# Kernel tuning notes

Hardware: AMD Instinct MI355X
Metric: run time of the kernel (lower is better)

Reference implementation:

```python
import jax, jax.numpy as jnp
import numpy as np


def conv1d(x, w, b, pad):
    # x: (B, Cin, T), w: (Cout, Cin, K), b: (Cout,)
    y = jax.lax.conv_general_dilated(x, w, window_strides=(1,), padding=[(pad, pad)],
                                     dimension_numbers=('NCH', 'OIH', 'NCH'))
    return y + b[None, :, None]


def setup_inputs() -> dict:
    key = jax.random.key(0)
    ks = jax.random.split(key, 12)
    B, Cm, T1, Ct, T2, Ca = 8, 80, 800, 512, 200, 80
    queries = jax.random.normal(ks[0], (B, Cm, T1), dtype=jnp.float32)
    keys = jax.random.normal(ks[1], (B, Ct, T2), dtype=jnp.float32)
    query_lens = jnp.full((B,), T1, dtype=jnp.int32)
    key_lens = jax.random.randint(ks[2], (B,), T2 // 2, T2 + 1)
    # mask True where key position is padding (>= key_len): (B, T2, 1)
    mask = (jnp.arange(T2)[None, :] >= key_lens[:, None])[:, :, None]
    attn_prior = jax.random.uniform(ks[3], (B, T1, T2), dtype=jnp.float32) + 0.1
    # key_proj: Conv1d(512->1024, k=3, pad=1) + ReLU + Conv1d(1024->80, k=1)
    kp_w1 = jax.random.normal(ks[4], (2 * Ct, Ct, 3), jnp.float32) * 0.02
    kp_b1 = jnp.zeros((2 * Ct,), jnp.float32)
    kp_w2 = jax.random.normal(ks[5], (Ca, 2 * Ct, 1), jnp.float32) * 0.02
    kp_b2 = jnp.zeros((Ca,), jnp.float32)
    # query_proj (3xconv): Conv1d(80->160,k3)+ReLU+Conv1d(160->80,k1)+ReLU+Conv1d(80->80,k1)
    qp_w1 = jax.random.normal(ks[6], (2 * Cm, Cm, 3), jnp.float32) * 0.05
    qp_b1 = jnp.zeros((2 * Cm,), jnp.float32)
    qp_w2 = jax.random.normal(ks[7], (Cm, 2 * Cm, 1), jnp.float32) * 0.05
    qp_b2 = jnp.zeros((Cm,), jnp.float32)
    qp_w3 = jax.random.normal(ks[8], (Ca, Cm, 1), jnp.float32) * 0.05
    qp_b3 = jnp.zeros((Ca,), jnp.float32)
    return {"queries": queries, "keys": keys, "query_lens": query_lens, "mask": mask,
            "attn_prior": attn_prior, "kp_w1": kp_w1, "kp_b1": kp_b1, "kp_w2": kp_w2,
            "kp_b2": kp_b2, "qp_w1": qp_w1, "qp_b1": qp_b1, "qp_w2": qp_w2,
            "qp_b2": qp_b2, "qp_w3": qp_w3, "qp_b3": qp_b3}


def reference(queries, keys, query_lens, mask, attn_prior,
              kp_w1, kp_b1, kp_w2, kp_b2,
              qp_w1, qp_b1, qp_w2, qp_b2, qp_w3, qp_b3):
    # key projection: (B, Ct, T2) -> (B, Ca, T2)
    ke = conv1d(keys, kp_w1, kp_b1, pad=1)
    ke = jax.nn.relu(ke)
    ke = conv1d(ke, kp_w2, kp_b2, pad=0)
    # query projection ('3xconv'): (B, Cm, T1) -> (B, Ca, T1)
    qe = conv1d(queries, qp_w1, qp_b1, pad=1)
    qe = jax.nn.relu(qe)
    qe = conv1d(qe, qp_w2, qp_b2, pad=0)
    qe = jax.nn.relu(qe)
    qe = conv1d(qe, qp_w3, qp_b3, pad=0)
    # broadcasted squared L2 distance: (B, Ca, T1, T2) -> reduce C -> (B, 1, T1, T2)
    diff2 = (qe[:, :, :, None] - ke[:, :, None, :]) ** 2
    attn = -0.0005 * jnp.sum(diff2, axis=1, keepdims=True)
    # prior in log domain
    attn = jax.nn.log_softmax(attn, axis=3) + jnp.log(attn_prior[:, None] + 1e-8)
    attn_logprob = attn
    # mask (B, T2, 1) -> (B, 1, 1, T2)
    m = jnp.transpose(mask, (0, 2, 1))[:, :, None, :]
    attn = jnp.where(m, -jnp.inf, attn)
    attn = jax.nn.softmax(attn, axis=3)
    return (attn, attn_logprob)
```

## Files before the change

### kernel.cpp

```cpp
#include <hip/hip_runtime.h>
#include <hip/hip_bf16.h>
#include <math.h>

#define B_  8
#define CM  80
#define T1_ 800
#define CT  512
#define T2_ 200
#define CA  80

using bf16 = __hip_bfloat16;
typedef __attribute__((ext_vector_type(8))) short bf16x8;
typedef __attribute__((ext_vector_type(4))) float f32x4;

#define LDSW 56
#define LDSW2 72
#define LDSW3 168
#define LDSW4 104

__device__ __forceinline__ float load_sel(const void* p, long idx, int isf32) {
  if (isf32) return ((const float*)p)[idx];
  return __bfloat162float(((const bf16*)p)[idx]);
}

__device__ __forceinline__ unsigned short f2bf(float x) {
  bf16 h = __float2bfloat16(x);
  return *reinterpret_cast<unsigned short*>(&h);
}

__device__ __forceinline__ int detect_f32(const unsigned short* q) {
  __shared__ int s_f;
  const int tid = threadIdx.x;
  if (tid < 64) {
    unsigned short u = q[2 * tid];
    int e = (u >> 7) & 0xFF;
    unsigned long long bal = __ballot(e < 100 || e > 154);
    if (tid == 0) s_f = (__popcll(bal) >= 16) ? 1 : 0;
  }
  __syncthreads();
  return s_f;
}

__device__ void task_cvt_t(const void* X, bf16* XT, int f, int C, int T,
                           int id2, int tilesT, float* smem, int tid) {
  const int per_b = tilesT * ((C + 31) >> 5);
  const int b = id2 / per_b;
  const int r = id2 - b * per_b;
  const int ct = r / tilesT, tt = r - ct * tilesT;
  const int c0 = ct * 32, t0 = tt * 32;
  const int tx = tid & 31, trow = tid >> 5;
#pragma unroll
  for (int p = 0; p < 4; ++p) {
    const int cr = trow + 8 * p;
    if (c0 + cr < C && t0 + tx < T)
      smem[cr * 33 + tx] = load_sel(X, ((long)b * C + c0 + cr) * T + t0 + tx, f);
  }
  __syncthreads();
#pragma unroll
  for (int p = 0; p < 4; ++p) {
    const int tr = trow + 8 * p;
    if (t0 + tr < T && c0 + tx < C)
      XT[((long)b * T + t0 + tr) * C + c0 + tx] =
          __float2bfloat16(smem[tx * 33 + tr]);
  }
}

__device__ void task_wfrag(const void* W, bf16* WF, int f, int id2, int tid) {
  const int id = id2 * 256 + tid;
  const int l  = id & 63;
  int rest = id >> 6;
  const int h  = rest & 1; rest >>= 1;
  const int mi = rest & 3; rest >>= 2;
  const int w2 = rest & 1; rest >>= 1;
  const int ks = rest % 24;
  const int p  = rest / 24;
  const int co = p * 128 + w2 * 64 + mi * 16 + (l & 15);
  const int k0 = ks * 64 + h * 32 + (l >> 4) * 8;
  const int dk = k0 >> 9;
  const int ci = k0 & 511;
  const long sbase = ((long)co * 512 + ci) * 3 + dk;
  ushort4 u0, u1;
  u0.x = f2bf(load_sel(W, sbase + 0 * 3, f));
  u0.y = f2bf(load_sel(W, sbase + 1 * 3, f));
  u0.z = f2bf(load_sel(W, sbase + 2 * 3, f));
  u0.w = f2bf(load_sel(W, sbase + 3 * 3, f));
  u1.x = f2bf(load_sel(W, sbase + 4 * 3, f));
  u1.y = f2bf(load_sel(W, sbase + 5 * 3, f));
  u1.z = f2bf(load_sel(W, sbase + 6 * 3, f));
  u1.w = f2bf(load_sel(W, sbase + 7 * 3, f));
  *(ushort4*)(WF + (long)id * 8) = u0;
  *(ushort4*)(WF + (long)id * 8 + 4) = u1;
}

__device__ void task_wt3v(const void* W, bf16* WT, int f, int Co, int Ci,
                          int id2, int tid) {
  const int i = id2 * 256 + tid;
  const int g4 = Ci >> 2;
  if (i >= Co * g4) return;
  const int co = i / g4, ci = (i - co * g4) * 4;
  const long sbase = ((long)co * Ci + ci) * 3;
  float w[12];
  if (f) {
    const float4* s = (const float4*)((const float*)W + sbase);
    float4 f0 = s[0], f1 = s[1], f2 = s[2];
    w[0]=f0.x; w[1]=f0.y; w[2]=f0.z; w[3]=f0.w; w[4]=f1.x; w[5]=f1.y;
    w[6]=f1.z; w[7]=f1.w; w[8]=f2.x; w[9]=f2.y; w[10]=f2.z; w[11]=f2.w;
  } else {
#pragma unroll
    for (int j = 0; j < 12; ++j) w[j] = load_sel(W, sbase + j, 0);
  }
#pragma unroll
  for (int dk = 0; dk < 3; ++dk) {
    ushort4 u;
    u.x = f2bf(w[0 * 3 + dk]); u.y = f2bf(w[1 * 3 + dk]);
    u.z = f2bf(w[2 * 3 + dk]); u.w = f2bf(w[3 * 3 + dk]);
    *(ushort4*)(WT + ((long)dk * Co + co) * Ci + ci) = u;
  }
}

__device__ void task_cvtv(const void* W, bf16* O, int f, int n, int id2, int tid) {
  const int i = (id2 * 256 + tid) * 4;
  if (i >= n) return;
  ushort4 u;
  if (f) {
    float4 v = *(const float4*)((const float*)W + i);
    u.x = f2bf(v.x); u.y = f2bf(v.y); u.z = f2bf(v.z); u.w = f2bf(v.w);
  } else {
    u.x = f2bf(load_sel(W, i, 0));     u.y = f2bf(load_sel(W, i + 1, 0));
    u.z = f2bf(load_sel(W, i + 2, 0)); u.w = f2bf(load_sel(W, i + 3, 0));
  }
  *(ushort4*)(O + i) = u;
}

__global__ __launch_bounds__(256) void k_prep(
    const void* __restrict__ queries, const void* __restrict__ keys,
    const void* __restrict__ mask,
    const void* __restrict__ kp_w1, const void* __restrict__ kp_b1,
    const void* __restrict__ kp_w2, const void* __restrict__ kp_b2,
    const void* __restrict__ qp_w1, const void* __restrict__ qp_b1,
    const void* __restrict__ qp_w2, const void* __restrict__ qp_b2,
    const void* __restrict__ qp_w3, const void* __restrict__ qp_b3,
    bf16* __restrict__ keysT, bf16* __restrict__ queriesT,
    bf16* __restrict__ w1F, bf16* __restrict__ qw1T,
    bf16* __restrict__ kw2c, bf16* __restrict__ qw2c, bf16* __restrict__ qw3c,
    float* __restrict__ biasf, float* __restrict__ mf, float* __restrict__ kn) {
  __shared__ float smem[32 * 33];
  const int tid = threadIdx.x;
  const int f = detect_f32((const unsigned short*)queries);
  int id = blockIdx.x;

  if (id < 896) { task_cvt_t(keys, keysT, f, CT, T2_, id, 7, smem, tid); return; }
  id -= 896;
  if (id < 600) { task_cvt_t(queries, queriesT, f, CM, T1_, id, 25, smem, tid); return; }
  id -= 600;
  if (id < 768) { task_wfrag(kp_w1, w1F, f, id, tid); return; }
  id -= 768;
  if (id < 13) { task_wt3v(qp_w1, qw1T, f, 160, CM, id, tid); return; }
  id -= 13;
  if (id < 80) { task_cvtv(kp_w2, kw2c, f, 80 * 1024, id, tid); return; }
  id -= 80;
  if (id < 13) { task_cvtv(qp_w2, qw2c, f, 80 * 160, id, tid); return; }
  id -= 13;
  if (id < 7) { task_cvtv(qp_w3, qw3c, f, 80 * 80, id, tid); return; }
  id -= 7;

  if (id == 0) {
    for (int i = tid; i < 1424; i += 256) {
      float v;
      if (i < 1024)      v = load_sel(kp_b1, i, f);
      else if (i < 1104) v = load_sel(kp_b2, i - 1024, f);
      else if (i < 1264) v = load_sel(qp_b1, i - 1104, f);
      else if (i < 1344) v = load_sel(qp_b2, i - 1264, f);
      else               v = load_sel(qp_b3, i - 1344, f);
      biasf[i] = v;
    }
    for (int i = tid; i < B_ * T2_; i += 256) kn[i] = 0.f;
    return;
  }

  {
    int* s_fmt = (int*)smem;
    const int nmask = B_ * T2_;
    if (tid == 0) s_fmt[0] = 1;
    __syncthreads();
    const unsigned int* wi = (const unsigned int*)mask;
    const int nw = nmask / 4;
    int pri = 0;
    for (int i = tid; i < nw; i += 256) {
      unsigned int w = wi[i];
      if (w == 0u || w == 1u) continue;
      if (w == 0x3F803F80u || w == 0x00003F80u) { pri = max(pri, 2); continue; }
      if (w == 0x3F800000u) continue;
      unsigned int b0 = w & 0xFFu, b1 = (w >> 8) & 0xFFu,
                   b2 = (w >> 16) & 0xFFu, b3 = (w >> 24) & 0xFFu;
      if (b0 <= 1u && b1 <= 1u && b2 <= 1u && b3 <= 1u) pri = max(pri, 3);
      else pri = max(pri, 2);
    }
    if (pri) atomicMax(&s_fmt[0], pri);
    __syncthreads();
    const int fmt = s_fmt[0];
    for (int i = tid; i < nmask; i += 256) {
      int m;
      if (fmt == 3)      m = ((const unsigned char*)mask)[i] != 0;
      else if (fmt == 2) m = ((const unsigned short*)mask)[i] != 0;
      else               m = (wi[i] != 0u);
      mf[i] = (float)m;
    }
  }
}

__device__ void conv_tile(
    const bf16* __restrict__ XT, const bf16* __restrict__ WT,
    const float* __restrict__ bias, void* __restrict__ Y,
    int Cin, int Cout, int T, int KW, int pad, int relu, int outmode,
    int m0, int n0, short* As, short* Bs, float* Y2 = nullptr) {
  const int K = Cin * KW;
  const int tid = threadIdx.x;
  const int wave = tid >> 6;
  const int lane = tid & 63;

  const int row = tid >> 2;
  const int koff = (tid & 3) * 8;
  const int n = n0 + row;
  const int bb = n / T;
  const int t = n - bb * T;

  const int wm = (wave >> 1) * 32;
  const int wn = (wave & 1) * 32;
  const int fm = lane & 15;
  const int quad = lane >> 4;

  f32x4 acc[2][2] = {};

  const short* ap0 = As + (wm + fm) * LDSW + quad * 8;
  const short* bp0 = Bs + (wn + fm) * LDSW + quad * 8;

  auto loadA = [&](int k0) -> uint4 {
    const int k = k0 + koff;
    const int m = m0 + row;
    uint4 v = {0u, 0u, 0u, 0u};
    if (m < Cout && k < K) {
      const int dk = k / Cin;
      const int ci = k - dk * Cin;
      v = *(const uint4*)(WT + ((long)dk * Cout + m) * Cin + ci);
    }
    return v;
  };
  auto loadB = [&](int k0) -> uint4 {
    const int k = k0 + koff;
    uint4 v = {0u, 0u, 0u, 0u};
    if (k < K) {
      const int dk = k / Cin;
      const int ci = k - dk * Cin;
      const int tt = t + dk - pad;
      if (tt >= 0 && tt < T)
        v = *(const uint4*)(XT + ((long)bb * T + tt) * Cin + ci);
    }
    return v;
  };

  uint4 va = loadA(0);
  uint4 vb = loadB(0);

  for (int k0 = 0; k0 < K; k0 += 32) {
    *(uint4*)(As + row * LDSW + koff) = va;
    *(uint4*)(Bs + row * LDSW + koff) = vb;
    if (k0 + 32 < K) {
      va = loadA(k0 + 32);
      vb = loadB(k0 + 32);
    }
    __syncthreads();
    {
      bf16x8 a0 = *(const bf16x8*)(ap0);
      bf16x8 a1 = *(const bf16x8*)(ap0 + 16 * LDSW);
      bf16x8 b0 = *(const bf16x8*)(bp0);
      bf16x8 b1 = *(const bf16x8*)(bp0 + 16 * LDSW);
      acc[0][0] = __builtin_amdgcn_mfma_f32_16x16x32_bf16(a0, b0, acc[0][0], 0, 0, 0);
      acc[0][1] = __builtin_amdgcn_mfma_f32_16x16x32_bf16(a0, b1, acc[0][1], 0, 0, 0);
      acc[1][0] = __builtin_amdgcn_mfma_f32_16x16x32_bf16(a1, b0, acc[1][0], 0, 0, 0);
      acc[1][1] = __builtin_amdgcn_mfma_f32_16x16x32_bf16(a1, b1, acc[1][1], 0, 0, 0);
    }
    __syncthreads();
  }

#pragma unroll
  for (int mi = 0; mi < 2; ++mi) {
    const int mrow = m0 + wm + mi * 16 + quad * 4;
    if (mrow >= Cout) continue;
    float bi[4];
#pragma unroll
    for (int r = 0; r < 4; ++r) bi[r] = bias[mrow + r];
#pragma unroll
    for (int ni = 0; ni < 2; ++ni) {
      const int ncol = n0 + wn + ni * 16 + fm;
      float o[4];
#pragma unroll
      for (int r = 0; r < 4; ++r) {
        float v = acc[mi][ni][r] + bi[r];
        if (relu) v = fmaxf(v, 0.f);
        o[r] = v;
      }
      if (outmode == 0) {
        ushort4 u;
        u.x = f2bf(o[0]); u.y = f2bf(o[1]); u.z = f2bf(o[2]); u.w = f2bf(o[3]);
        *(ushort4*)((bf16*)Y + (long)ncol * Cout + mrow) = u;
      } else if (outmode == 1) {
        *(float4*)((float*)Y + (long)ncol * Cout + mrow) =
            make_float4(o[0], o[1], o[2], o[3]);
      } else {
        const int bb2 = ncol / T;
        const int tloc = ncol - bb2 * T;
        float s4 = 0.f;
#pragma unroll
        for (int r = 0; r < 4; ++r) {
          ((float*)Y)[((long)bb2 * Cout + mrow + r) * T + tloc] = -2.f * o[r];
          s4 = fmaf(o[r], o[r], s4);
        }
        atomicAdd(&Y2[ncol], s4);
      }
    }
  }
}

__device__ void conv_key128(
    const bf16* __restrict__ XT, const bf16* __restrict__ WF,
    const float* __restrict__ bias, bf16* __restrict__ Y,
    int panel, int n0, short* Bs) {
  const int Cin = CT, Cout = 1024, T = T2_;
  const int tid = threadIdx.x;
  const int wave = tid >> 6;
  const int lane = tid & 63;
  const int m0 = panel * 128;

  const int rowb = tid >> 2;
  const int nb = n0 + rowb;
  const int bbb = nb / T;
  const int tb = nb - bbb * T;
  const int kcb = (tid & 3) * 16;

  const int w2 = wave >> 1;
  const int wm = w2 * 64;
  const int wn = (wave & 1) * 32;
  const int fm = lane & 15;
  const int quad = lane >> 4;

  f32x4 acc[4][2] = {};
  const short* bp0 = Bs + (wn + fm) * LDSW2 + quad * 8;

  uint4 vb0, vb1;
  auto loadB = [&](int k0) {
    const int dk = k0 >> 9;
    const int ci0 = k0 & 511;
    const int tt = tb + dk - 1;
    if (tt >= 0 && tt < T) {
      const bf16* src = XT + ((long)bbb * T + tt) * Cin + ci0 + kcb;
      vb0 = *(const uint4*)(src);
      vb1 = *(const uint4*)(src + 8);
    } else {
      uint4 z = {0u, 0u, 0u, 0u};
      vb0 = z; vb1 = z;
    }
  };

  loadB(0);

  for (int k0 = 0; k0 < 1536; k0 += 64) {
    const int ks = k0 >> 6;
    {
      short* dstb = Bs + rowb * LDSW2 + kcb;
      *(uint4*)(dstb) = vb0;
      *(uint4*)(dstb + 8) = vb1;
    }
    if (k0 + 64 < 1536) loadB(k0 + 64);

    const long abase = ((((long)panel * 24 + ks) * 2 + w2) * 4096) + lane * 8;
    bf16x8 a[4][2];
#pragma unroll
    for (int mi = 0; mi < 4; ++mi)
#pragma unroll
      for (int h = 0; h < 2; ++h)
        a[mi][h] = *(const bf16x8*)(WF + abase + (mi * 2 + h) * 512);

    __syncthreads();
#pragma unroll
    for (int h = 0; h < 2; ++h) {
      bf16x8 b0 = *(const bf16x8*)(bp0 + h * 32);
      bf16x8 b1 = *(const bf16x8*)(bp0 + 16 * LDSW2 + h * 32);
#pragma unroll
      for (int mi = 0; mi < 4; ++mi) {
        acc[mi][0] = __builtin_amdgcn_mfma_f32_16x16x32_bf16(a[mi][h], b0, acc[mi][0], 0, 0, 0);
        acc[mi][1] = __builtin_amdgcn_mfma_f32_16x16x32_bf16(a[mi][h], b1, acc[mi][1], 0, 0, 0);
      }
    }
    __syncthreads();
  }

#pragma unroll
  for (int mi = 0; mi < 4; ++mi) {
    const int mrow = m0 + wm + mi * 16 + quad * 4;
    float bi[4];
#pragma unroll
    for (int r = 0; r < 4; ++r) bi[r] = bias[mrow + r];
#pragma unroll
    for (int ni = 0; ni < 2; ++ni) {
      const int ncol = n0 + wn + ni * 16 + fm;
      const long base = (long)ncol * Cout + mrow;
      ushort4 u;
      u.x = f2bf(fmaxf(acc[mi][ni][0] + bi[0], 0.f));
      u.y = f2bf(fmaxf(acc[mi][ni][1] + bi[1], 0.f));
      u.z = f2bf(fmaxf(acc[mi][ni][2] + bi[2], 0.f));
      u.w = f2bf(fmaxf(acc[mi][ni][3] + bi[3], 0.f));
      *(ushort4*)(Y + base) = u;
    }
  }
}

__global__ __launch_bounds__(256) void k_conv1(
    const bf16* __restrict__ keysT, const bf16* __restrict__ w1F,
    const float* __restrict__ b_k1, bf16* __restrict__ ke1T,
    const bf16* __restrict__ queriesT, const bf16* __restrict__ qw1T,
    const float* __restrict__ b_q1, bf16* __restrict__ qe1T) {
  __shared__ __align__(16) short smem[2 * 64 * LDSW];
  int j = blockIdx.x;
  if (j < 200) {
    conv_key128(keysT, w1F, b_k1, ke1T, j & 7, (j >> 3) * 64, smem);
  } else {
    j -= 200;
    conv_tile(queriesT, qw1T, b_q1, qe1T, CM, 160, T1_, 3, 1, 1, 0,
              (j / 100) * 64, (j % 100) * 64, smem, smem + 64 * LDSW);
  }
}

__device__ void conv23_tile(
    const bf16* __restrict__ qe1T, const bf16* __restrict__ qw2c,
    const float* __restrict__ b_q2, const bf16* __restrict__ qw3c,
    const float* __restrict__ b_q3, float* __restrict__ qeT,
    float* __restrict__ qn, int n0, short* smem) {
  short* sIn = smem;
  short* sW2 = smem + 64 * LDSW3;
  short* sC  = smem;
  short* sW3 = smem + 64 * LDSW3;
  const int tid = threadIdx.x;
  const int wave = tid >> 6;
  const int lane = tid & 63;
  const int fm = lane & 15;
  const int quad = lane >> 4;

#pragma unroll
  for (int c = tid; c < 1280; c += 256) {
    const int row = c / 20, kc = (c - row * 20) * 8;
    uint4 v = *(const uint4*)(qe1T + (long)(n0 + row) * 160 + kc);
    *(uint4*)(sIn + row * LDSW3 + kc) = v;
  }
  for (int c = tid; c < 1600; c += 256) {
    const int row = c / 20, kc = (c - row * 20) * 8;
    uint4 v = *(const uint4*)(qw2c + (long)row * 160 + kc);
    *(uint4*)(sW2 + row * LDSW3 + kc) = v;
  }
  __syncthreads();

  f32x4 acc1[5] = {};
#pragma unroll
  for (int ks = 0; ks < 5; ++ks) {
    bf16x8 b = *(const bf16x8*)(sIn + (16 * wave + fm) * LDSW3 + ks * 32 + quad * 8);
#pragma unroll
    for (int mt = 0; mt < 5; ++mt) {
      bf16x8 a = *(const bf16x8*)(sW2 + (16 * mt + fm) * LDSW3 + ks * 32 + quad * 8);
      acc1[mt] = __builtin_amdgcn_mfma_f32_16x16x32_bf16(a, b, acc1[mt], 0, 0, 0);
    }
  }
  __syncthreads();

#pragma unroll
  for (int mt = 0; mt < 5; ++mt) {
    const int ch = 16 * mt + quad * 4;
    const float4 b2 = *(const float4*)(b_q2 + ch);
    ushort4 u;
    u.x = f2bf(fmaxf(acc1[mt][0] + b2.x, 0.f));
    u.y = f2bf(fmaxf(acc1[mt][1] + b2.y, 0.f));
    u.z = f2bf(fmaxf(acc1[mt][2] + b2.z, 0.f));
    u.w = f2bf(fmaxf(acc1[mt][3] + b2.w, 0.f));
    *(ushort4*)(sC + (16 * wave + fm) * LDSW4 + ch) = u;
  }
  if (tid < 128) {
    const int row = tid >> 1, off = 80 + (tid & 1) * 8;
    uint4 z = {0u, 0u, 0u, 0u};
    *(uint4*)(sC + row * LDSW4 + off) = z;
  }
  for (int c = tid; c < 800; c += 256) {
    const int row = c / 10, kc = (c - row * 10) * 8;
    uint4 v = *(const uint4*)(qw3c + (long)row * 80 + kc);
    *(uint4*)(sW3 + row * LDSW4 + kc) = v;
  }
  if (tid < 160) {
    const int row = tid >> 1, off = 80 + (tid & 1) * 8;
    uint4 z = {0u, 0u, 0u, 0u};
    *(uint4*)(sW3 + row * LDSW4 + off) = z;
  }
  __syncthreads();

  f32x4 acc2[5] = {};
#pragma unroll
  for (int ks = 0; ks < 3; ++ks) {
    bf16x8 b = *(const bf16x8*)(sC + (16 * wave + fm) * LDSW4 + ks * 32 + quad * 8);
#pragma unroll
    for (int mt = 0; mt < 5; ++mt) {
      bf16x8 a = *(const bf16x8*)(sW3 + (16 * mt + fm) * LDSW4 + ks * 32 + quad * 8);
      acc2[mt] = __builtin_amdgcn_mfma_f32_16x16x32_bf16(a, b, acc2[mt], 0, 0, 0);
    }
  }

  const int pos = n0 + 16 * wave + fm;
  float p = 0.f;
#pragma unroll
  for (int mt = 0; mt < 5; ++mt) {
    const int ch = 16 * mt + quad * 4;
    const float4 b3 = *(const float4*)(b_q3 + ch);
    float4 o = make_float4(acc2[mt][0] + b3.x, acc2[mt][1] + b3.y,
                           acc2[mt][2] + b3.z, acc2[mt][3] + b3.w);
    p = fmaf(o.x, o.x, p); p = fmaf(o.y, o.y, p);
    p = fmaf(o.z, o.z, p); p = fmaf(o.w, o.w, p);
    *(float4*)(qeT + (long)pos * CA + ch) = o;
  }
  p += __shfl_xor(p, 16, 64);
  p += __shfl_xor(p, 32, 64);
  if (quad == 0) qn[pos] = p;
}

__global__ __launch_bounds__(256) void k_conv2f(
    const bf16* __restrict__ ke1T, const bf16* __restrict__ kw2c,
    const float* __restrict__ b_k2, float* __restrict__ keT,
    float* __restrict__ kn,
    const bf16* __restrict__ qe1T, const bf16* __restrict__ qw2c,
    const float* __restrict__ b_q2, const bf16* __restrict__ qw3c,
    const float* __restrict__ b_q3, float* __restrict__ qeT,
    float* __restrict__ qn) {
  __shared__ __align__(16) short smem[64 * LDSW3 + 80 * LDSW3];
  int j = blockIdx.x;
  if (j < 50) {
    conv_tile(ke1T, kw2c, b_k2, keT, 1024, CA, T2_, 1, 0, 0, 2,
              (j / 25) * 64, (j % 25) * 64, smem, smem + 64 * LDSW, kn);
  } else {
    conv23_tile(qe1T, qw2c, b_q2, qw3c, b_q3, qeT, qn, (j - 50) * 64, smem);
  }
}

__global__ __launch_bounds__(256) void k_dist(
    const float* __restrict__ qeT, const float* __restrict__ keT2,
    const float* __restrict__ kn, const float* __restrict__ qn,
    const void* __restrict__ prior, const float* __restrict__ mf,
    void* __restrict__ out, const unsigned short* __restrict__ qprobe) {
  __shared__ float sq[4 * CA];
  __shared__ float sqn[4];
  __shared__ float redA[16], redB[16], redC[16], redD[16];
  const int f = detect_f32(qprobe);
  const int b = blockIdx.y;
  const int t1base = blockIdx.x * 4;
  const int tid = threadIdx.x;
  const int wid = tid >> 6;

  for (int i = tid; i < 4 * CA; i += 256) {
    int u = i / CA, c = i - u * CA;
    sq[i] = qeT[((long)b * T1_ + t1base + u) * CA + c];
  }
  if (tid < 4) sqn[tid] = qn[b * T1_ + t1base + tid];
  __syncthreads();

  const int t2 = tid;
  const bool valid = (t2 < T2_);
  float x[4] = {-INFINITY, -INFINITY, -INFINITY, -INFINITY};
  if (valid) {
    const float* kp = keT2 + (long)b * CA * T2_ + t2;
    const float knv = kn[b * T2_ + t2];
    float a0 = 0.f, a1 = 0.f, a2 = 0.f, a3 = 0.f;
#pragma unroll 2
    for (int j = 0; j < CA; j += 4) {
      const float4 q0 = *(const float4*)(sq + 0 * CA + j);
      const float4 q1 = *(const float4*)(sq + 1 * CA + j);
      const float4 q2 = *(const float4*)(sq + 2 * CA + j);
      const float4 q3 = *(const float4*)(sq + 3 * CA + j);
      const float k0v = kp[(j + 0) * T2_];
      const float k1v = kp[(j + 1) * T2_];
      const float k2v = kp[(j + 2) * T2_];
      const float k3v = kp[(j + 3) * T2_];
      a0 = fmaf(k0v, q0.x, a0); a0 = fmaf(k1v, q0.y, a0);
      a0 = fmaf(k2v, q0.z, a0); a0 = fmaf(k3v, q0.w, a0);
      a1 = fmaf(k0v, q1.x, a1); a1 = fmaf(k1v, q1.y, a1);
      a1 = fmaf(k2v, q1.z, a1); a1 = fmaf(k3v, q1.w, a1);
      a2 = fmaf(k0v, q2.x, a2); a2 = fmaf(k1v, q2.y, a2);
      a2 = fmaf(k2v, q2.z, a2); a2 = fmaf(k3v, q2.w, a2);
      a3 = fmaf(k0v, q3.x, a3); a3 = fmaf(k1v, q3.y, a3);
      a3 = fmaf(k2v, q3.z, a3); a3 = fmaf(k3v, q3.w, a3);
    }
    x[0] = -0.0005f * (a0 + sqn[0] + knv);
    x[1] = -0.0005f * (a1 + sqn[1] + knv);
    x[2] = -0.0005f * (a2 + sqn[2] + knv);
    x[3] = -0.0005f * (a3 + sqn[3] + knv);
  }

  const float mval = valid ? mf[b * T2_ + t2] : 0.f;
  const long N = (long)B_ * T1_ * T2_;

  float m[4] = {x[0], x[1], x[2], x[3]};
#pragma unroll
  for (int o = 32; o > 0; o >>= 1)
#pragma unroll
    for (int u = 0; u < 4; ++u) m[u] = fmaxf(m[u], __shfl_down(m[u], o, 64));
  if ((tid & 63) == 0)
#pragma unroll
    for (int u = 0; u < 4; ++u) redA[wid * 4 + u] = m[u];
  __syncthreads();
  float M1[4];
#pragma unroll
  for (int u = 0; u < 4; ++u)
    M1[u] = fmaxf(fmaxf(redA[u], redA[4 + u]), fmaxf(redA[8 + u], redA[12 + u]));

  float e[4], s1[4];
#pragma unroll
  for (int u = 0; u < 4; ++u) {
    e[u] = (x[u] == -INFINITY) ? 0.f : __expf(x[u] - M1[u]);
    s1[u] = e[u];
  }
#pragma unroll
  for (int o = 32; o > 0; o >>= 1)
#pragma unroll
    for (int u = 0; u < 4; ++u) s1[u] += __shfl_down(s1[u], o, 64);
  if ((tid & 63) == 0)
#pragma unroll
    for (int u = 0; u < 4; ++u) redB[wid * 4 + u] = s1[u];
  __syncthreads();
  float lp[4];
#pragma unroll
  for (int u = 0; u < 4; ++u) {
    const float S1 = redB[u] + redB[4 + u] + redB[8 + u] + redB[12 + u];
    const float logZ = __logf(S1);
    lp[u] = -INFINITY;
    if (valid) {
      const long oidx = ((long)b * T1_ + t1base + u) * T2_ + t2;
      float pr = load_sel(prior, oidx, f);
      lp[u] = (x[u] - M1[u] - logZ) + __logf(fmaxf(pr, 0.f) + 1e-8f);
      if (f) ((float*)out)[N + oidx] = lp[u];
      else   ((bf16*)out)[N + oidx] = __float2bfloat16(lp[u]);
    }
  }

  float xm[4], m2[4];
#pragma unroll
  for (int u = 0; u < 4; ++u) {
    xm[u] = (valid && mval != 0.f) ? -INFINITY : lp[u];
    m2[u] = xm[u];
  }
#pragma unroll
  for (int o = 32; o > 0; o >>= 1)
#pragma unroll
    for (int u = 0; u < 4; ++u) m2[u] = fmaxf(m2[u], __shfl_down(m2[u], o, 64));
  if ((tid & 63) == 0)
#pragma unroll
    for (int u = 0; u < 4; ++u) redC[wid * 4 + u] = m2[u];
  __syncthreads();
  float M2[4];
#pragma unroll
  for (int u = 0; u < 4; ++u)
    M2[u] = fmaxf(fmaxf(redC[u], redC[4 + u]), fmaxf(redC[8 + u], redC[12 + u]));

  float e2[4], s2[4];
#pragma unroll
  for (int u = 0; u < 4; ++u) {
    e2[u] = (xm[u] == -INFINITY) ? 0.f : __expf(xm[u] - M2[u]);
    s2[u] = e2[u];
  }
#pragma unroll
  for (int o = 32; o > 0; o >>= 1)
#pragma unroll
    for (int u = 0; u < 4; ++u) s2[u] += __shfl_down(s2[u], o, 64);
  if ((tid & 63) == 0)
#pragma unroll
    for (int u = 0; u < 4; ++u) redD[wid * 4 + u] = s2[u];
  __syncthreads();
#pragma unroll
  for (int u = 0; u < 4; ++u) {
    const float S2 = redD[u] + redD[4 + u] + redD[8 + u] + redD[12 + u];
    if (valid) {
      float a = (S2 > 0.f) ? (e2[u] / S2) : 0.f;
      const long oidx = ((long)b * T1_ + t1base + u) * T2_ + t2;
      if (f) ((float*)out)[oidx] = a;
      else   ((bf16*)out)[oidx] = __float2bfloat16(a);
    }
  }
}

extern "C" void kernel_launch(void* const* d_in, const int* in_sizes, int n_in,
                              void* d_out, int out_size, void* d_ws, size_t ws_size,
                              hipStream_t stream) {
  const void* queries = d_in[0];
  const void* keys    = d_in[1];
  const void* mask    = d_in[3];
  const void* prior   = d_in[4];
  const void* kp_w1 = d_in[5];
  const void* kp_b1 = d_in[6];
  const void* kp_w2 = d_in[7];
  const void* kp_b2 = d_in[8];
  const void* qp_w1 = d_in[9];
  const void* qp_b1 = d_in[10];
  const void* qp_w2 = d_in[11];
  const void* qp_b2 = d_in[12];
  const void* qp_w3 = d_in[13];
  const void* qp_b3 = d_in[14];

  float* keT   = (float*)d_ws;
  float* qeT   = keT + 128000;
  float* mf    = qeT + 512000;
  float* biasf = mf + 1600;
  float* kn    = biasf + 1440;
  float* qn    = kn + 1600;
  bf16* keysT    = (bf16*)(qn + 6400);
  bf16* queriesT = keysT + 819200;
  bf16* w1F      = queriesT + 512000;
  bf16* qw1T     = w1F + 1572864;
  bf16* kw2c     = qw1T + 38400;
  bf16* qw2c     = kw2c + 81920;
  bf16* qw3c     = qw2c + 12800;
  bf16* ke1T     = qw3c + 6400;
  bf16* qe1T     = ke1T + 1638400;

  float* b_k1 = biasf;
  float* b_k2 = biasf + 1024;
  float* b_q1 = biasf + 1104;
  float* b_q2 = biasf + 1264;
  float* b_q3 = biasf + 1344;

  k_prep<<<2379, 256, 0, stream>>>(
      queries, keys, mask,
      kp_w1, kp_b1, kp_w2, kp_b2,
      qp_w1, qp_b1, qp_w2, qp_b2, qp_w3, qp_b3,
      keysT, queriesT, w1F, qw1T, kw2c, qw2c, qw3c, biasf, mf, kn);

  k_conv1<<<500, 256, 0, stream>>>(keysT, w1F, b_k1, ke1T,
                                   queriesT, qw1T, b_q1, qe1T);

  k_conv2f<<<150, 256, 0, stream>>>(ke1T, kw2c, b_k2, keT, kn,
                                    qe1T, qw2c, b_q2, qw3c, b_q3, qeT, qn);

  k_dist<<<dim3(200, B_), 256, 0, stream>>>(
      qeT, keT, kn, qn, prior, mf, d_out, (const unsigned short*)queries);
}
```

Baseline: 150.8 us.

## Prefetch weight fragments across K-steps and merge softmax reductions in dist kernel

In the key conv GEMM, the A (weight) fragments for the next K-step are now loaded into a second register set while the current step's MFMAs run, overlapping global loads with compute at the cost of extra VGPRs. In the distance kernel, the prior and mask loads move to the start of the kernel. The second softmax is rewritten algebraically: its logsumexp shift cancels, so it runs on x plus log-prior directly. This lets the two max reductions and the two sum reductions each run together, cutting the block barriers from four to two. The change risks register pressure in the conv kernel and slight numerical differences in the softmax.

```diff
diff --git a/kernel.cpp b/kernel.cpp
--- a/kernel.cpp
+++ b/kernel.cpp
@@ -339,7 +339,6 @@
   const int kcb = (tid & 3) * 16;
 
   const int w2 = wave >> 1;
-  const int wm = w2 * 64;
   const int wn = (wave & 1) * 32;
   const int fm = lane & 15;
   const int quad = lane >> 4;
@@ -362,42 +361,57 @@
     }
   };
 
+  bf16x8 a0c[4], a1c[4], a0n[4], a1n[4];
+  auto loadA = [&](int ks, bf16x8 d0[4], bf16x8 d1[4]) {
+    const long abase = ((((long)panel * 24 + ks) * 2 + w2) * 4096) + lane * 8;
+#pragma unroll
+    for (int mi = 0; mi < 4; ++mi) {
+      d0[mi] = *(const bf16x8*)(WF + abase + (mi * 2 + 0) * 512);
+      d1[mi] = *(const bf16x8*)(WF + abase + (mi * 2 + 1) * 512);
+    }
+  };
+
   loadB(0);
+  loadA(0, a0c, a1c);
 
   for (int k0 = 0; k0 < 1536; k0 += 64) {
-    const int ks = k0 >> 6;
     {
       short* dstb = Bs + rowb * LDSW2 + kcb;
       *(uint4*)(dstb) = vb0;
       *(uint4*)(dstb + 8) = vb1;
     }
-    if (k0 + 64 < 1536) loadB(k0 + 64);
-
-    const long abase = ((((long)panel * 24 + ks) * 2 + w2) * 4096) + lane * 8;
-    bf16x8 a[4][2];
-#pragma unroll
-    for (int mi = 0; mi < 4; ++mi)
-#pragma unroll
-      for (int h = 0; h < 2; ++h)
-        a[mi][h] = *(const bf16x8*)(WF + abase + (mi * 2 + h) * 512);
-
+    const bool more = (k0 + 64 < 1536);
+    if (more) {
+      loadB(k0 + 64);
+      loadA((k0 >> 6) + 1, a0n, a1n);
+    }
     __syncthreads();
-#pragma unroll
-    for (int h = 0; h < 2; ++h) {
-      bf16x8 b0 = *(const bf16x8*)(bp0 + h * 32);
-      bf16x8 b1 = *(const bf16x8*)(bp0 + 16 * LDSW2 + h * 32);
+    {
+      bf16x8 b00 = *(const bf16x8*)(bp0);
+      bf16x8 b01 = *(const bf16x8*)(bp0 + 16 * LDSW2);
 #pragma unroll
       for (int mi = 0; mi < 4; ++mi) {
-        acc[mi][0] = __builtin_amdgcn_mfma_f32_16x16x32_bf16(a[mi][h], b0, acc[mi][0], 0, 0, 0);
-        acc[mi][1] = __builtin_amdgcn_mfma_f32_16x16x32_bf16(a[mi][h], b1, acc[mi][1], 0, 0, 0);
+        acc[mi][0] = __builtin_amdgcn_mfma_f32_16x16x32_bf16(a0c[mi], b00, acc[mi][0], 0, 0, 0);
+        acc[mi][1] = __builtin_amdgcn_mfma_f32_16x16x32_bf16(a0c[mi], b01, acc[mi][1], 0, 0, 0);
       }
+      bf16x8 b10 = *(const bf16x8*)(bp0 + 32);
+      bf16x8 b11 = *(const bf16x8*)(bp0 + 16 * LDSW2 + 32);
+#pragma unroll
+      for (int mi = 0; mi < 4; ++mi) {
+        acc[mi][0] = __builtin_amdgcn_mfma_f32_16x16x32_bf16(a1c[mi], b10, acc[mi][0], 0, 0, 0);
+        acc[mi][1] = __builtin_amdgcn_mfma_f32_16x16x32_bf16(a1c[mi], b11, acc[mi][1], 0, 0, 0);
+      }
     }
     __syncthreads();
+    if (more) {
+#pragma unroll
+      for (int mi = 0; mi < 4; ++mi) { a0c[mi] = a0n[mi]; a1c[mi] = a1n[mi]; }
+    }
   }
 
 #pragma unroll
   for (int mi = 0; mi < 4; ++mi) {
-    const int mrow = m0 + wm + mi * 16 + quad * 4;
+    const int mrow = m0 + w2 * 64 + mi * 16 + quad * 4;
     float bi[4];
 #pragma unroll
     for (int r = 0; r < 4; ++r) bi[r] = bias[mrow + r];
@@ -559,6 +573,19 @@
   const int tid = threadIdx.x;
   const int wid = tid >> 6;
 
+  const int t2 = tid;
+  const bool valid = (t2 < T2_);
+  const long N = (long)B_ * T1_ * T2_;
+
+  float pr[4] = {0.f, 0.f, 0.f, 0.f};
+  float mval = 1.f;
+  if (valid) {
+#pragma unroll
+    for (int u = 0; u < 4; ++u)
+      pr[u] = load_sel(prior, ((long)b * T1_ + t1base + u) * T2_ + t2, f);
+    mval = mf[b * T2_ + t2];
+  }
+
   for (int i = tid; i < 4 * CA; i += 256) {
     int u = i / CA, c = i - u * CA;
     sq[i] = qeT[((long)b * T1_ + t1base + u) * CA + c];
@@ -566,8 +593,6 @@
   if (tid < 4) sqn[tid] = qn[b * T1_ + t1base + tid];
   __syncthreads();
 
-  const int t2 = tid;
-  const bool valid = (t2 < T2_);
   float x[4] = {-INFINITY, -INFINITY, -INFINITY, -INFINITY};
   if (valid) {
     const float* kp = keT2 + (long)b * CA * T2_ + t2;
@@ -598,93 +623,80 @@
     x[3] = -0.0005f * (a3 + sqn[3] + knv);
   }
 
-  const float mval = valid ? mf[b * T2_ + t2] : 0.f;
-  const long N = (long)B_ * T1_ * T2_;
-
-  float m[4] = {x[0], x[1], x[2], x[3]};
+  float y[4], ym[4];
+#pragma unroll
+  for (int u = 0; u < 4; ++u) {
+    if (valid) {
+      const float lpr = __logf(fmaxf(pr[u], 0.f) + 1e-8f);
+      y[u] = x[u] + lpr;
+    } else {
+      y[u] = -INFINITY;
+    }
+    ym[u] = (valid && mval == 0.f) ? y[u] : -INFINITY;
+  }
+
+  float m1[4], m2[4];
+#pragma unroll
+  for (int u = 0; u < 4; ++u) { m1[u] = x[u]; m2[u] = ym[u]; }
 #pragma unroll
   for (int o = 32; o > 0; o >>= 1)
 #pragma unroll
-    for (int u = 0; u < 4; ++u) m[u] = fmaxf(m[u], __shfl_down(m[u], o, 64));
+    for (int u = 0; u < 4; ++u) {
+      m1[u] = fmaxf(m1[u], __shfl_down(m1[u], o, 64));
+      m2[u] = fmaxf(m2[u], __shfl_down(m2[u], o, 64));
+    }
   if ((tid & 63) == 0)
 #pragma unroll
-    for (int u = 0; u < 4; ++u) redA[wid * 4 + u] = m[u];
+    for (int u = 0; u < 4; ++u) {
+      redA[wid * 4 + u] = m1[u];
+      redB[wid * 4 + u] = m2[u];
+    }
   __syncthreads();
-  float M1[4];
-#pragma unroll
-  for (int u = 0; u < 4; ++u)
+  float M1[4], M2[4];
+#pragma unroll
+  for (int u = 0; u < 4; ++u) {
     M1[u] = fmaxf(fmaxf(redA[u], redA[4 + u]), fmaxf(redA[8 + u], redA[12 + u]));
-
-  float e[4], s1[4];
+    M2[u] = fmaxf(fmaxf(redB[u], redB[4 + u]), fmaxf(redB[8 + u], redB[12 + u]));
+  }
+
+  float e2[4], s1[4], s2[4];
 #pragma unroll
   for (int u = 0; u < 4; ++u) {
-    e[u] = (x[u] == -INFINITY) ? 0.f : __expf(x[u] - M1[u]);
-    s1[u] = e[u];
+    s1[u] = (x[u] == -INFINITY) ? 0.f : __expf(x[u] - M1[u]);
+    e2[u] = (ym[u] == -INFINITY) ? 0.f : __expf(ym[u] - M2[u]);
+    s2[u] = e2[u];
   }
 #pragma unroll
   for (int o = 32; o > 0; o >>= 1)
 #pragma unroll
-    for (int u = 0; u < 4; ++u) s1[u] += __shfl_down(s1[u], o, 64);
+    for (int u = 0; u < 4; ++u) {
+      s1[u] += __shfl_down(s1[u], o, 64);
+      s2[u] += __shfl_down(s2[u], o, 64);
+    }
   if ((tid & 63) == 0)
 #pragma unroll
-    for (int u = 0; u < 4; ++u) redB[wid * 4 + u] = s1[u];
+    for (int u = 0; u < 4; ++u) {
+      redC[wid * 4 + u] = s1[u];
+      redD[wid * 4 + u] = s2[u];
+    }
   __syncthreads();
-  float lp[4];
+
 #pragma unroll
   for (int u = 0; u < 4; ++u) {
-    const float S1 = redB[u] + redB[4 + u] + redB[8 + u] + redB[12 + u];
-    const float logZ = __logf(S1);
-    lp[u] = -INFINITY;
-    if (valid) {
-      const long oidx = ((long)b * T1_ + t1base + u) * T2_ + t2;
-      float pr = load_sel(prior, oidx, f);
-      lp[u] = (x[u] - M1[u] - logZ) + __logf(fmaxf(pr, 0.f) + 1e-8f);
-      if (f) ((float*)out)[N + oidx] = lp[u];
-      else   ((bf16*)out)[N + oidx] = __float2bfloat16(lp[u]);
-    }
-  }
-
-  float xm[4], m2[4];
-#pragma unroll
-  for (int u = 0; u < 4; ++u) {
-    xm[u] = (valid && mval != 0.f) ? -INFINITY : lp[u];
-    m2[u] = xm[u];
-  }
-#pragma unroll
-  for (int o = 32; o > 0; o >>= 1)
-#pragma unroll
-    for (int u = 0; u < 4; ++u) m2[u] = fmaxf(m2[u], __shfl_down(m2[u], o, 64));
-  if ((tid & 63) == 0)
-#pragma unroll
-    for (int u = 0; u < 4; ++u) redC[wid * 4 + u] = m2[u];
-  __syncthreads();
-  float M2[4];
-#pragma unroll
-  for (int u = 0; u < 4; ++u)
-    M2[u] = fmaxf(fmaxf(redC[u], redC[4 + u]), fmaxf(redC[8 + u], redC[12 + u]));
-
-  float e2[4], s2[4];
-#pragma unroll
-  for (int u = 0; u < 4; ++u) {
-    e2[u] = (xm[u] == -INFINITY) ? 0.f : __expf(xm[u] - M2[u]);
-    s2[u] = e2[u];
-  }
-#pragma unroll
-  for (int o = 32; o > 0; o >>= 1)
-#pragma unroll
-    for (int u = 0; u < 4; ++u) s2[u] += __shfl_down(s2[u], o, 64);
-  if ((tid & 63) == 0)
-#pragma unroll
-    for (int u = 0; u < 4; ++u) redD[wid * 4 + u] = s2[u];
-  __syncthreads();
-#pragma unroll
-  for (int u = 0; u < 4; ++u) {
+    const float S1 = redC[u] + redC[4 + u] + redC[8 + u] + redC[12 + u];
     const float S2 = redD[u] + redD[4 + u] + redD[8 + u] + redD[12 + u];
     if (valid) {
-      float a = (S2 > 0.f) ? (e2[u] / S2) : 0.f;
+      const float logZ = __logf(S1);
+      const float lp = y[u] - M1[u] - logZ;
+      const float a = (S2 > 0.f) ? (e2[u] / S2) : 0.f;
       const long oidx = ((long)b * T1_ + t1base + u) * T2_ + t2;
-      if (f) ((float*)out)[oidx] = a;
-      else   ((bf16*)out)[oidx] = __float2bfloat16(a);
+      if (f) {
+        ((float*)out)[N + oidx] = lp;
+        ((float*)out)[oidx] = a;
+      } else {
+        ((bf16*)out)[N + oidx] = __float2bfloat16(lp);
+        ((bf16*)out)[oidx] = __float2bfloat16(a);
+      }
     }
   }
 }
```

New measurement: 148.1 us. No clear change (-1.8%).
